# Performance work log

Hardware: AMD Instinct MI355X
Metric: run time of the kernel (lower is better)

Reference implementation:

```python
import jax, jax.numpy as jnp
import numpy as np

B, T9, N, C = 2048, 9, 62, 10   # batch, graph_num, node_num, dim_in
TT = 8                           # conv steps t=1..8
D = 62                           # TLSGCN dim_out (== node_num, required by GRU input_size)
ED = 3                           # emb_dim
K = 2                            # link_len
P = 100                          # zigzag persistence-image side
H = 62                           # GRU hidden size (BGI dim_out)


def setup_inputs() -> dict:
    key = jax.random.key(0)
    ks = jax.random.split(key, 12)
    s = 0.1
    return {
        "x": jax.random.normal(ks[0], (B, T9, N, C), jnp.float32),
        "zigzag_PI": jax.random.uniform(ks[1], (B, P, P), dtype=jnp.float32),
        "node_embeddings": jax.random.normal(ks[2], (N, ED), jnp.float32),
        "Wp": jax.random.normal(ks[3], (TT, ED, K, C, D), jnp.float32) * s,
        "bp": jax.random.normal(ks[4], (TT, ED, D), jnp.float32) * s,
        "Tparam": jax.random.normal(ks[5], (TT, T9), jnp.float32),
        "Wz": jax.random.normal(ks[6], (TT, P * P), jnp.float32) * 0.01,
        "W_ih": jax.random.normal(ks[7], (3 * H, D), jnp.float32) * s,
        "W_hh": jax.random.normal(ks[8], (3 * H, H), jnp.float32) * s,
        "b_ih": jnp.zeros((3 * H,), jnp.float32),
        "b_hh": jnp.zeros((3 * H,), jnp.float32),
        "W1": jax.random.normal(ks[9], (256, N), jnp.float32) * s,
        "b1": jnp.zeros((256,), jnp.float32),
        "W2": jax.random.normal(ks[10], (3, 256), jnp.float32) * s,
        "b2": jnp.zeros((3,), jnp.float32),
    }


def reference(x, zigzag_PI, node_embeddings, Wp, bp, Tparam, Wz,
              W_ih, W_hh, b_ih, b_hh, W1, b1, W2, b2):
    # --- TLSGCN graph diffusion conv, vectorized over the 8 per-step modules ---
    A = jax.nn.softmax(jax.nn.relu(node_embeddings @ node_embeddings.T), axis=1)  # [N,N]
    S = jnp.stack([jnp.eye(N, dtype=x.dtype), A], axis=0)                          # [K,N,N]
    w = jnp.einsum('ne,tekco->tnkco', node_embeddings, Wp)                         # [TT,N,K,C,D]
    b = jnp.einsum('ne,teo->tno', node_embeddings, bp)                             # [TT,N,D]
    xg = jnp.einsum('knm,btmc->btknc', S, x[:, 1:, :, :])                          # [B,TT,K,N,C]
    x_gconv = jnp.einsum('btknc,tnkco->btno', xg, w) + b[None]                     # [B,TT,N,D]
    # temporal window: step t attends over its first t frames (window_len = t)
    tmask = jnp.arange(T9)[None, :] < jnp.arange(1, TT + 1)[:, None]               # [TT,T9]
    alpha = jax.nn.softmax(jnp.where(tmask, Tparam, -jnp.inf), axis=1)             # [TT,T9]
    xw = jnp.einsum('bsnc,ts->btnc', x, alpha)                                     # [B,TT,N,C]
    x_wconv = jnp.einsum('btnc,tnco->btno', xw, w[:, :, 0])                        # [B,TT,N,D]
    # zigzag persistence-image topological gate (per step)
    zz = jax.nn.sigmoid(jnp.einsum('bp,tp->bt', zigzag_PI.reshape(B, -1), Wz))     # [B,TT]
    h = zz[:, :, None, None] * x_gconv + x_wconv                                   # [B,TT,N,D]
    h = jnp.where(jnp.isnan(h) | jnp.isinf(h), jnp.zeros((), h.dtype), h)
    # --- shared GRU applied per node: fold nodes into the batch dim ---
    seq = h.transpose(1, 0, 2, 3).reshape(TT, B * N, D)                            # [TT, B*N, D]

    def cell(hprev, xt):
        gi = xt @ W_ih.T + b_ih
        gh = hprev @ W_hh.T + b_hh
        ir, iz, inn = jnp.split(gi, 3, axis=-1)
        hr, hz, hn = jnp.split(gh, 3, axis=-1)
        r = jax.nn.sigmoid(ir + hr)
        zg = jax.nn.sigmoid(iz + hz)
        ng = jnp.tanh(inn + r * hn)
        hnew = (1.0 - zg) * ng + zg * hprev
        return hnew, None

    h0 = jnp.zeros((B * N, H), seq.dtype)
    hT, _ = jax.lax.scan(cell, h0, seq)        # final hidden == output at last step
    out = hT.reshape(B, N, H).sum(axis=2)      # [B, N]
    out = jax.nn.relu(out @ W1.T + b1)         # [B, 256]
    out = jax.nn.relu(out @ W2.T + b2)         # [B, 3]
    return out
```

## Files before the change

### kernel.cpp

```cpp
#include <hip/hip_runtime.h>

typedef unsigned short u16;
typedef _Float16 f16;
typedef __attribute__((ext_vector_type(8))) _Float16 h8v;
typedef __attribute__((ext_vector_type(4))) float f4v;

#define SC_RZ (-1.44269504f)
#define SC_N  (2.88539008f)

__device__ __forceinline__ u16 f2h_bits(float f){
  f16 h = (f16)f;
  return __builtin_bit_cast(u16, h);
}
__device__ __forceinline__ float sigmf(float x){
  return __builtin_amdgcn_rcpf(1.f + __expf(-x));
}

__global__ __launch_bounds__(64) void k_prepA(
    const float* __restrict__ E, const float* __restrict__ Tp,
    float* __restrict__ A, float* __restrict__ alpha)
{
  const int n = blockIdx.x, tid = threadIdx.x;
  if (n < 62){
    float e0 = E[n*3], e1 = E[n*3+1], e2 = E[n*3+2];
    float s = -1e30f;
    if (tid < 62){
      float d = e0*E[tid*3] + e1*E[tid*3+1] + e2*E[tid*3+2];
      s = d > 0.f ? d : 0.f;
    }
    float mx = s;
    #pragma unroll
    for (int off = 1; off < 64; off <<= 1) mx = fmaxf(mx, __shfl_xor(mx, off));
    float e = (tid < 62) ? __expf(s - mx) : 0.f;
    float sum = e;
    #pragma unroll
    for (int off = 1; off < 64; off <<= 1) sum += __shfl_xor(sum, off);
    if (tid < 62) A[n*62 + tid] = e / sum;
  } else {
    if (tid < 8){
      int t = tid;
      float mx = -1e30f;
      for (int s = 0; s <= t; ++s) mx = fmaxf(mx, Tp[t*9+s]);
      float sum = 0.f;
      for (int s = 0; s <= t; ++s) sum += __expf(Tp[t*9+s] - mx);
      float inv = 1.f / sum;
      for (int s = 0; s < 9; ++s)
        alpha[t*9+s] = (s <= t) ? __expf(Tp[t*9+s] - mx) * inv : 0.f;
    }
  }
}

__global__ __launch_bounds__(256) void k_wpad(
    const float* __restrict__ Whh, const float* __restrict__ bih,
    const float* __restrict__ bhh, u16* __restrict__ WhhH)
{
  int i = blockIdx.x*256 + threadIdx.x;
  if (i >= 12288) return;
  int row = i >> 6, k = i & 63, g = row >> 6, jj = row & 63;
  float sc = (g == 2) ? SC_N : SC_RZ;
  float vh = 0.f;
  if (jj < 62){
    if (k < 62) vh = Whh[(g*62+jj)*62 + k];
    else if (k == 62) vh = (g < 2) ? (bih[g*62+jj] + bhh[g*62+jj]) : bhh[124+jj];
  }
  WhhH[i] = f2h_bits(vh * sc);
}

__global__ __launch_bounds__(256) void k_m2(
    const float* __restrict__ E, const float* __restrict__ Wp,
    const float* __restrict__ bp, const float* __restrict__ Wih,
    const float* __restrict__ bih, u16* __restrict__ M2)
{
  const int bid = blockIdx.x;
  const int t = bid / 62, n = bid % 62, tid = threadIdx.x;
  __shared__ float w2s[1240];
  __shared__ float bias[62];
  const float e0 = E[n*3], e1 = E[n*3+1], e2 = E[n*3+2];
  for (int i = tid; i < 1240; i += 256){
    int o = i / 20, k = i % 20, c = k >> 1, kl = k & 1;
    w2s[i] = e0*Wp[(((t*3+0)*2+kl)*10+c)*62 + o]
           + e1*Wp[(((t*3+1)*2+kl)*10+c)*62 + o]
           + e2*Wp[(((t*3+2)*2+kl)*10+c)*62 + o];
  }
  if (tid < 62)
    bias[tid] = e0*bp[(t*3+0)*62+tid] + e1*bp[(t*3+1)*62+tid]
              + e2*bp[(t*3+2)*62+tid];
  __syncthreads();
  for (int i = tid; i < 3072; i += 256){
    int col = i >> 4, d = i & 15, g = col >> 6, jj = col & 63;
    float sc = (g == 2) ? SC_N : SC_RZ;
    unsigned outw = 0;
    if (jj < 62){
      const float* wr = Wih + (g*62+jj)*62;
      if (d < 10){
        int k0 = 2*d;
        float v0 = 0.f, v1 = 0.f;
        for (int o = 0; o < 62; ++o){
          float w = wr[o];
          v0 += w * w2s[o*20 + k0];
          v1 += w * w2s[o*20 + k0 + 1];
        }
        outw = (unsigned)f2h_bits(v0*sc) | ((unsigned)f2h_bits(v1*sc) << 16);
      } else if (d == 10){
        float v0 = 0.f;
        for (int o = 0; o < 62; ++o) v0 += wr[o]*bias[o];
        float v1 = (g == 2) ? bih[124+jj] : 0.f;
        outw = (unsigned)f2h_bits(v0*sc) | ((unsigned)f2h_bits(v1*sc) << 16);
      }
    }
    ((unsigned*)M2)[((size_t)bid*192 + col)*16 + d] = outw;
  }
}

__global__ __launch_bounds__(256) void k_zz(
    const float* __restrict__ PI, const float* __restrict__ Wz,
    float* __restrict__ zzO)
{
  const int b0 = blockIdx.x*4, tid = threadIdx.x;
  float acc[32];
  #pragma unroll
  for (int i = 0; i < 32; ++i) acc[i] = 0.f;
  const float4* p0 = (const float4*)(PI + (size_t)(b0+0)*10000);
  const float4* p1 = (const float4*)(PI + (size_t)(b0+1)*10000);
  const float4* p2 = (const float4*)(PI + (size_t)(b0+2)*10000);
  const float4* p3 = (const float4*)(PI + (size_t)(b0+3)*10000);
  const float4* wz4 = (const float4*)Wz;
  for (int p = tid; p < 2500; p += 256){
    float4 x0 = p0[p], x1 = p1[p], x2 = p2[p], x3 = p3[p];
    #pragma unroll
    for (int t = 0; t < 8; ++t){
      float4 w = wz4[t*2500 + p];
      acc[t*4+0] += x0.x*w.x + x0.y*w.y + x0.z*w.z + x0.w*w.w;
      acc[t*4+1] += x1.x*w.x + x1.y*w.y + x1.z*w.z + x1.w*w.w;
      acc[t*4+2] += x2.x*w.x + x2.y*w.y + x2.z*w.z + x2.w*w.w;
      acc[t*4+3] += x3.x*w.x + x3.y*w.y + x3.z*w.z + x3.w*w.w;
    }
  }
  __shared__ float red[128];
  int lane = tid & 63, wid = tid >> 6;
  #pragma unroll
  for (int i = 0; i < 32; ++i){
    float v = acc[i];
    v += __shfl_xor(v, 1);  v += __shfl_xor(v, 2);  v += __shfl_xor(v, 4);
    v += __shfl_xor(v, 8);  v += __shfl_xor(v, 16); v += __shfl_xor(v, 32);
    if (lane == 0) red[i*4 + wid] = v;
  }
  __syncthreads();
  if (tid < 32){
    float s = red[tid*4] + red[tid*4+1] + red[tid*4+2] + red[tid*4+3];
    int t = tid >> 2, bq = tid & 3;
    zzO[t*2048 + b0 + bq] = sigmf(s);
  }
}

__global__ __launch_bounds__(256) void k_u(
    const float* __restrict__ x, const float* __restrict__ A,
    const float* __restrict__ alpha, const float* __restrict__ zz,
    u16* __restrict__ U01)
{
  const int b = blockIdx.x, tid = threadIdx.x;
  __shared__ float xs[5580];
  __shared__ f16 xT[80*72];
  __shared__ f16 A16[64*72];
  __shared__ f16 xg[64*80];
  __shared__ float al[72];
  __shared__ float zzb[8];

  const float* pxb = x + (size_t)b*5580;
  const float4* px4 = (const float4*)pxb;
  for (int i = tid; i < 1395; i += 256) ((float4*)xs)[i] = px4[i];
  for (int i = tid; i < 3844; i += 256){
    int n = i / 62, m = i % 62;
    A16[n*72 + m] = (f16)A[i];
  }
  for (int i = tid; i < 640; i += 256) A16[(i/10)*72 + 62 + (i%10)] = (f16)0.f;
  for (int i = tid; i < 124; i += 256) A16[(62 + i/62)*72 + (i%62)] = (f16)0.f;
  for (int i = tid; i < 4960; i += 256){
    int s1 = i / 620, r = i % 620, m = r / 10, c = r % 10;
    xT[(s1*10 + c)*72 + m] = (f16)pxb[620 + i];
  }
  for (int i = tid; i < 800; i += 256) xT[(i/10)*72 + 62 + (i%10)] = (f16)0.f;
  if (tid < 72) al[tid] = alpha[tid];
  if (tid < 8) zzb[tid] = zz[tid*2048 + b];
  __syncthreads();

  {
    const int w_id = tid >> 6, lane = tid & 63, ln = lane & 15, hi = lane >> 4;
    h8v af0 = *(const h8v*)&A16[(w_id*16 + ln)*72 + hi*8];
    h8v af1 = *(const h8v*)&A16[(w_id*16 + ln)*72 + 32 + hi*8];
    f4v Z4 = {0.f, 0.f, 0.f, 0.f};
    #pragma unroll
    for (int Nt = 0; Nt < 5; ++Nt){
      h8v bf0 = *(const h8v*)&xT[(Nt*16 + ln)*72 + hi*8];
      h8v bf1 = *(const h8v*)&xT[(Nt*16 + ln)*72 + 32 + hi*8];
      f4v acc = __builtin_amdgcn_mfma_f32_16x16x32_f16(af0, bf0, Z4, 0,0,0);
      acc = __builtin_amdgcn_mfma_f32_16x16x32_f16(af1, bf1, acc, 0,0,0);
      #pragma unroll
      for (int rg = 0; rg < 4; ++rg)
        xg[(w_id*16 + hi*4 + rg)*80 + Nt*16 + ln] = (f16)acc[rg];
    }
  }
  __syncthreads();

  const int t = tid >> 5, nq = (tid >> 1) & 15, ch = tid & 1;
  const int n0 = nq*4, c0 = ch*5;
  float alr[9];
  #pragma unroll
  for (int s = 0; s < 9; ++s) alr[s] = al[t*9+s];
  const float z = zzb[t];
  const unsigned zpack = (unsigned)f2h_bits(z) | (0x3C00u << 16);
  #pragma unroll
  for (int i = 0; i < 4; ++i){
    int n = n0 + i;
    if (n < 62){
      unsigned pk[5];
      #pragma unroll
      for (int c = 0; c < 5; ++c){
        int cc = c0 + c;
        float xw = 0.f;
        #pragma unroll
        for (int s = 0; s < 9; ++s) xw += alr[s]*xs[s*620 + n*10 + cc];
        float u0 = z*xs[(t+1)*620 + n*10 + cc] + xw;
        float u1 = z*(float)xg[n*80 + t*10 + cc];
        pk[c] = (unsigned)f2h_bits(u0) | ((unsigned)f2h_bits(u1) << 16);
      }
      unsigned* dst = (unsigned*)(U01 + ((size_t)(t*62 + n)*2048 + b)*32);
      #pragma unroll
      for (int c = 0; c < 5; ++c) dst[c0 + c] = pk[c];
      if (ch == 0){ dst[10] = zpack; dst[12] = 0; dst[13] = 0; }
      else        { dst[11] = 0;     dst[14] = 0; dst[15] = 0; }
    }
  }
}

__global__ __launch_bounds__(256, 3) void k_gru(
    const u16* __restrict__ U01, const u16* __restrict__ M2,
    const u16* __restrict__ WhhH, float* __restrict__ outSum)
{
  __shared__ f16 Hs[2][32*72];
  __shared__ float red[128];

  const int tid = threadIdx.x;
  int bid = blockIdx.x;
  bid = (bid & 7)*496 + (bid >> 3);
  const int n_idx = bid >> 6;
  const int b0 = (bid & 63) << 5;
  const int lane = tid & 63;
  const int w_id = tid >> 6;
  const int ln = lane & 15;
  const int hi = lane >> 4;
  const int j = w_id*16 + ln;

  h8v whhF[3][2];
  #pragma unroll
  for (int g = 0; g < 3; ++g)
    #pragma unroll
    for (int ks = 0; ks < 2; ++ks)
      whhF[g][ks] = *(const h8v*)(const void*)(WhhH + (g*64 + j)*64 + ks*32 + hi*8);

  for (int i = tid; i < 2304; i += 256){
    f16 v = ((i % 72) == 62) ? (f16)1.f : (f16)0.f;
    Hs[0][i] = v; Hs[1][i] = v;
  }

  const u16* pU = U01 + ((size_t)n_idx*2048 + b0)*32;
  const u16* pM = M2 + (size_t)n_idx*192*32;
  const int oU0 = ln*32 + hi*8;
  const int oU1 = (16 + ln)*32 + hi*8;
  const int oM0 = j*32 + hi*8;
  const int oM1 = (64 + j)*32 + hi*8;
  const int oM2 = (128 + j)*32 + hi*8;
  const size_t TSU = (size_t)62*2048*32;
  const size_t TSM = (size_t)62*192*32;

  h8v uA0 = *(const h8v*)(const void*)(pU + oU0);
  h8v uA1 = *(const h8v*)(const void*)(pU + oU1);
  h8v mA0 = *(const h8v*)(const void*)(pM + oM0);
  h8v mA1 = *(const h8v*)(const void*)(pM + oM1);
  h8v mA2 = *(const h8v*)(const void*)(pM + oM2);
  h8v uB0, uB1, mB0, mB1, mB2;

  float h_reg[8];
  #pragma unroll
  for (int i = 0; i < 8; ++i) h_reg[i] = 0.f;
  __syncthreads();

  const f4v Z4 = {0.f, 0.f, 0.f, 0.f};
  #pragma unroll
  for (int t = 0; t < 8; ++t){
    const int p = t & 1;
    if (t < 7){
      const u16* qU = pU + (size_t)(t+1)*TSU;
      const u16* qM = pM + (size_t)(t+1)*TSM;
      uB0 = *(const h8v*)(const void*)(qU + oU0);
      uB1 = *(const h8v*)(const void*)(qU + oU1);
      mB0 = *(const h8v*)(const void*)(qM + oM0);
      mB1 = *(const h8v*)(const void*)(qM + oM1);
      mB2 = *(const h8v*)(const void*)(qM + oM2);
    }
    h8v hf00 = *(const h8v*)&Hs[p][ln*72 + hi*8];
    h8v hf01 = *(const h8v*)&Hs[p][ln*72 + 32 + hi*8];
    h8v hf10 = *(const h8v*)&Hs[p][(16+ln)*72 + hi*8];
    h8v hf11 = *(const h8v*)&Hs[p][(16+ln)*72 + 32 + hi*8];

    f4v ar[2], az[2], axn[2], ahn[2];
    ar[0]  = __builtin_amdgcn_mfma_f32_16x16x32_f16(hf00, whhF[0][0], Z4, 0,0,0);
    ar[0]  = __builtin_amdgcn_mfma_f32_16x16x32_f16(hf01, whhF[0][1], ar[0], 0,0,0);
    ar[0]  = __builtin_amdgcn_mfma_f32_16x16x32_f16(uA0, mA0, ar[0], 0,0,0);
    ar[1]  = __builtin_amdgcn_mfma_f32_16x16x32_f16(hf10, whhF[0][0], Z4, 0,0,0);
    ar[1]  = __builtin_amdgcn_mfma_f32_16x16x32_f16(hf11, whhF[0][1], ar[1], 0,0,0);
    ar[1]  = __builtin_amdgcn_mfma_f32_16x16x32_f16(uA1, mA0, ar[1], 0,0,0);
    az[0]  = __builtin_amdgcn_mfma_f32_16x16x32_f16(hf00, whhF[1][0], Z4, 0,0,0);
    az[0]  = __builtin_amdgcn_mfma_f32_16x16x32_f16(hf01, whhF[1][1], az[0], 0,0,0);
    az[0]  = __builtin_amdgcn_mfma_f32_16x16x32_f16(uA0, mA1, az[0], 0,0,0);
    az[1]  = __builtin_amdgcn_mfma_f32_16x16x32_f16(hf10, whhF[1][0], Z4, 0,0,0);
    az[1]  = __builtin_amdgcn_mfma_f32_16x16x32_f16(hf11, whhF[1][1], az[1], 0,0,0);
    az[1]  = __builtin_amdgcn_mfma_f32_16x16x32_f16(uA1, mA1, az[1], 0,0,0);
    ahn[0] = __builtin_amdgcn_mfma_f32_16x16x32_f16(hf00, whhF[2][0], Z4, 0,0,0);
    ahn[0] = __builtin_amdgcn_mfma_f32_16x16x32_f16(hf01, whhF[2][1], ahn[0], 0,0,0);
    ahn[1] = __builtin_amdgcn_mfma_f32_16x16x32_f16(hf10, whhF[2][0], Z4, 0,0,0);
    ahn[1] = __builtin_amdgcn_mfma_f32_16x16x32_f16(hf11, whhF[2][1], ahn[1], 0,0,0);
    axn[0] = __builtin_amdgcn_mfma_f32_16x16x32_f16(uA0, mA2, Z4, 0,0,0);
    axn[1] = __builtin_amdgcn_mfma_f32_16x16x32_f16(uA1, mA2, Z4, 0,0,0);

    const bool last = (t == 7);
    #pragma unroll
    for (int mi = 0; mi < 2; ++mi)
      #pragma unroll
      for (int rg = 0; rg < 4; ++rg){
        float r  = __builtin_amdgcn_rcpf(1.f + exp2f(ar[mi][rg]));
        float zg = __builtin_amdgcn_rcpf(1.f + exp2f(az[mi][rg]));
        float yn = axn[mi][rg] + r*ahn[mi][rg];
        float ng = fmaf(-2.f, __builtin_amdgcn_rcpf(1.f + exp2f(yn)), 1.f);
        int idx = mi*4 + rg;
        float hnew = ng + zg*(h_reg[idx] - ng);
        h_reg[idx] = hnew;
        if (!last && j < 62)
          Hs[p^1][(mi*16 + hi*4 + rg)*72 + j] = (f16)hnew;
      }
    uA0 = uB0; uA1 = uB1; mA0 = mB0; mA1 = mB1; mA2 = mB2;
    __syncthreads();
  }

  #pragma unroll
  for (int mi = 0; mi < 2; ++mi)
    #pragma unroll
    for (int rg = 0; rg < 4; ++rg){
      float v = (j < 62) ? h_reg[mi*4 + rg] : 0.f;
      v += __shfl_xor(v, 1); v += __shfl_xor(v, 2);
      v += __shfl_xor(v, 4); v += __shfl_xor(v, 8);
      if (ln == 0) red[w_id*32 + mi*16 + hi*4 + rg] = v;
    }
  __syncthreads();
  if (tid < 32)
    outSum[(size_t)n_idx*2048 + b0 + tid] =
        red[tid] + red[32+tid] + red[64+tid] + red[96+tid];
}

__global__ __launch_bounds__(256) void k_mlp(
    const float* __restrict__ outSum,
    const float* __restrict__ W1, const float* __restrict__ b1,
    const float* __restrict__ W2, const float* __restrict__ b2,
    float* __restrict__ out)
{
  const int b0 = blockIdx.x*8, tid = threadIdx.x;
  __shared__ float W1s[15872];
  __shared__ float vec[8][62];
  __shared__ float o1[8][256];
  for (int i = tid; i < 15872; i += 256) W1s[i] = W1[i];
  for (int i = tid; i < 496; i += 256){
    int n = i >> 3, bl = i & 7;
    vec[bl][n] = outSum[(size_t)n*2048 + b0 + bl];
  }
  __syncthreads();
  {
    float a[8];
    #pragma unroll
    for (int bl = 0; bl < 8; ++bl) a[bl] = b1[tid];
    for (int n = 0; n < 62; ++n){
      float w = W1s[tid*62 + n];
      #pragma unroll
      for (int bl = 0; bl < 8; ++bl) a[bl] += w * vec[bl][n];
    }
    #pragma unroll
    for (int bl = 0; bl < 8; ++bl) o1[bl][tid] = fmaxf(a[bl], 0.f);
  }
  __syncthreads();
  if (tid < 24){
    int bl = tid / 3, o = tid % 3;
    float s = b2[o];
    for (int k = 0; k < 256; ++k) s += o1[bl][k]*W2[o*256 + k];
    out[(b0+bl)*3 + o] = fmaxf(s, 0.f);
  }
}

extern "C" void kernel_launch(void* const* d_in, const int* in_sizes, int n_in,
                              void* d_out, int out_size, void* d_ws, size_t ws_size,
                              hipStream_t stream)
{
  const float* x   = (const float*)d_in[0];
  const float* PI  = (const float*)d_in[1];
  const float* E   = (const float*)d_in[2];
  const float* Wp  = (const float*)d_in[3];
  const float* bp  = (const float*)d_in[4];
  const float* Tp  = (const float*)d_in[5];
  const float* Wz  = (const float*)d_in[6];
  const float* Wih = (const float*)d_in[7];
  const float* Whh = (const float*)d_in[8];
  const float* bih = (const float*)d_in[9];
  const float* bhh = (const float*)d_in[10];
  const float* W1  = (const float*)d_in[11];
  const float* b1  = (const float*)d_in[12];
  const float* W2  = (const float*)d_in[13];
  const float* b2  = (const float*)d_in[14];
  float* out = (float*)d_out;

  char* ws = (char*)d_ws;
  size_t off = 0;
  auto take = [&](size_t bytes)->char*{
    char* p = ws + off; off = (off + bytes + 255) & ~(size_t)255; return p;
  };
  float* pA     = (float*)take(3844*4);
  float* palpha = (float*)take(72*4);
  float* pzz    = (float*)take(16384*4);
  u16*   pWhhH  = (u16*)take(12288*2);
  u16*   pM2    = (u16*)take((size_t)496*192*32*2);
  u16*   pU01   = (u16*)take((size_t)496*2048*32*2);
  float* pos    = (float*)take((size_t)126976*4);

  k_prepA<<<63, 64, 0, stream>>>(E, Tp, pA, palpha);
  k_wpad<<<48, 256, 0, stream>>>(Whh, bih, bhh, pWhhH);
  k_m2<<<496, 256, 0, stream>>>(E, Wp, bp, Wih, bih, pM2);
  k_zz<<<512, 256, 0, stream>>>(PI, Wz, pzz);
  k_u<<<2048, 256, 0, stream>>>(x, pA, palpha, pzz, pU01);
  k_gru<<<3968, 256, 0, stream>>>(pU01, pM2, pWhhH, pos);
  k_mlp<<<256, 256, 0, stream>>>(pos, W1, b1, W2, b2, out);
}
```

Measured before the change: 204.8 us.

## Restructure GRU kernel to per-wave independent rows, drop block syncs, shrink U buffer

The GRU kernel is rewritten so each wave owns 16 batch rows and computes all 64 hidden outputs itself, with weights as the A operand. The hidden state now stays in per-wave LDS and in packed half registers, which removes the block-wide __syncthreads per timestep and the cross-wave reduction. The U01 staging buffer row stride drops from 32 to 24 halves to cut memory traffic, and the two prep kernels are merged into one launch. The cost is more registers (occupancy hint lowered to 2), M2 fragments reloaded each step, and the hidden state carried between steps in fp16 rather than fp32, which may change accuracy.

```diff
diff --git a/kernel.cpp b/kernel.cpp
--- a/kernel.cpp
+++ b/kernel.cpp
@@ -1,7 +1,9 @@
 #include <hip/hip_runtime.h>
 
 typedef unsigned short u16;
+typedef unsigned int u32;
 typedef _Float16 f16;
+typedef __attribute__((ext_vector_type(2))) _Float16 h2v;
 typedef __attribute__((ext_vector_type(8))) _Float16 h8v;
 typedef __attribute__((ext_vector_type(4))) float f4v;
 
@@ -16,27 +18,32 @@
   return __builtin_amdgcn_rcpf(1.f + __expf(-x));
 }
 
-__global__ __launch_bounds__(64) void k_prepA(
+__global__ __launch_bounds__(256) void k_prep(
     const float* __restrict__ E, const float* __restrict__ Tp,
-    float* __restrict__ A, float* __restrict__ alpha)
-{
-  const int n = blockIdx.x, tid = threadIdx.x;
-  if (n < 62){
-    float e0 = E[n*3], e1 = E[n*3+1], e2 = E[n*3+2];
-    float s = -1e30f;
-    if (tid < 62){
-      float d = e0*E[tid*3] + e1*E[tid*3+1] + e2*E[tid*3+2];
-      s = d > 0.f ? d : 0.f;
-    }
-    float mx = s;
-    #pragma unroll
-    for (int off = 1; off < 64; off <<= 1) mx = fmaxf(mx, __shfl_xor(mx, off));
-    float e = (tid < 62) ? __expf(s - mx) : 0.f;
-    float sum = e;
-    #pragma unroll
-    for (int off = 1; off < 64; off <<= 1) sum += __shfl_xor(sum, off);
-    if (tid < 62) A[n*62 + tid] = e / sum;
-  } else {
+    const float* __restrict__ Whh, const float* __restrict__ bih,
+    const float* __restrict__ bhh,
+    float* __restrict__ A, float* __restrict__ alpha, u16* __restrict__ WhhH)
+{
+  const int bid = blockIdx.x, tid = threadIdx.x;
+  if (bid < 62){
+    if (tid < 64){
+      const int n = bid;
+      float e0 = E[n*3], e1 = E[n*3+1], e2 = E[n*3+2];
+      float s = -1e30f;
+      if (tid < 62){
+        float d = e0*E[tid*3] + e1*E[tid*3+1] + e2*E[tid*3+2];
+        s = d > 0.f ? d : 0.f;
+      }
+      float mx = s;
+      #pragma unroll
+      for (int off = 1; off < 64; off <<= 1) mx = fmaxf(mx, __shfl_xor(mx, off));
+      float e = (tid < 62) ? __expf(s - mx) : 0.f;
+      float sum = e;
+      #pragma unroll
+      for (int off = 1; off < 64; off <<= 1) sum += __shfl_xor(sum, off);
+      if (tid < 62) A[n*62 + tid] = e / sum;
+    }
+  } else if (bid == 62){
     if (tid < 8){
       int t = tid;
       float mx = -1e30f;
@@ -47,23 +54,19 @@
       for (int s = 0; s < 9; ++s)
         alpha[t*9+s] = (s <= t) ? __expf(Tp[t*9+s] - mx) * inv : 0.f;
     }
-  }
-}
-
-__global__ __launch_bounds__(256) void k_wpad(
-    const float* __restrict__ Whh, const float* __restrict__ bih,
-    const float* __restrict__ bhh, u16* __restrict__ WhhH)
-{
-  int i = blockIdx.x*256 + threadIdx.x;
-  if (i >= 12288) return;
-  int row = i >> 6, k = i & 63, g = row >> 6, jj = row & 63;
-  float sc = (g == 2) ? SC_N : SC_RZ;
-  float vh = 0.f;
-  if (jj < 62){
-    if (k < 62) vh = Whh[(g*62+jj)*62 + k];
-    else if (k == 62) vh = (g < 2) ? (bih[g*62+jj] + bhh[g*62+jj]) : bhh[124+jj];
-  }
-  WhhH[i] = f2h_bits(vh * sc);
+  } else {
+    int i = (bid - 63)*256 + tid;
+    if (i < 12288){
+      int row = i >> 6, k = i & 63, g = row >> 6, jj = row & 63;
+      float sc = (g == 2) ? SC_N : SC_RZ;
+      float vh = 0.f;
+      if (jj < 62){
+        if (k < 62) vh = Whh[(g*62+jj)*62 + k];
+        else if (k == 62) vh = (g < 2) ? (bih[g*62+jj] + bhh[g*62+jj]) : bhh[124+jj];
+      }
+      WhhH[i] = f2h_bits(vh * sc);
+    }
+  }
 }
 
 __global__ __launch_bounds__(256) void k_m2(
@@ -224,137 +227,131 @@
         float u1 = z*(float)xg[n*80 + t*10 + cc];
         pk[c] = (unsigned)f2h_bits(u0) | ((unsigned)f2h_bits(u1) << 16);
       }
-      unsigned* dst = (unsigned*)(U01 + ((size_t)(t*62 + n)*2048 + b)*32);
+      unsigned* dst = (unsigned*)(U01 + ((size_t)(t*62 + n)*2048 + b)*24);
       #pragma unroll
       for (int c = 0; c < 5; ++c) dst[c0 + c] = pk[c];
-      if (ch == 0){ dst[10] = zpack; dst[12] = 0; dst[13] = 0; }
-      else        { dst[11] = 0;     dst[14] = 0; dst[15] = 0; }
-    }
-  }
-}
-
-__global__ __launch_bounds__(256, 3) void k_gru(
+      if (ch == 0) dst[10] = zpack; else dst[11] = 0;
+    }
+  }
+}
+
+__global__ __launch_bounds__(256, 2) void k_gru(
     const u16* __restrict__ U01, const u16* __restrict__ M2,
     const u16* __restrict__ WhhH, float* __restrict__ outSum)
 {
-  __shared__ f16 Hs[2][32*72];
-  __shared__ float red[128];
+  __shared__ f16 Ht[4][16*72];
 
   const int tid = threadIdx.x;
   int bid = blockIdx.x;
-  bid = (bid & 7)*496 + (bid >> 3);
-  const int n_idx = bid >> 6;
-  const int b0 = (bid & 63) << 5;
+  bid = (bid & 7)*248 + (bid >> 3);
+  const int n_idx = bid >> 5;
+  const int w_id = tid >> 6;
+  const int row0 = (bid & 31)*64 + w_id*16;
   const int lane = tid & 63;
-  const int w_id = tid >> 6;
   const int ln = lane & 15;
   const int hi = lane >> 4;
-  const int j = w_id*16 + ln;
-
-  h8v whhF[3][2];
+
+  f16* Hw = &Ht[w_id][0];
+
+  h8v whhA[3][4][2];
   #pragma unroll
   for (int g = 0; g < 3; ++g)
     #pragma unroll
-    for (int ks = 0; ks < 2; ++ks)
-      whhF[g][ks] = *(const h8v*)(const void*)(WhhH + (g*64 + j)*64 + ks*32 + hi*8);
-
-  for (int i = tid; i < 2304; i += 256){
-    f16 v = ((i % 72) == 62) ? (f16)1.f : (f16)0.f;
-    Hs[0][i] = v; Hs[1][i] = v;
-  }
-
-  const u16* pU = U01 + ((size_t)n_idx*2048 + b0)*32;
-  const u16* pM = M2 + (size_t)n_idx*192*32;
-  const int oU0 = ln*32 + hi*8;
-  const int oU1 = (16 + ln)*32 + hi*8;
-  const int oM0 = j*32 + hi*8;
-  const int oM1 = (64 + j)*32 + hi*8;
-  const int oM2 = (128 + j)*32 + hi*8;
-  const size_t TSU = (size_t)62*2048*32;
+    for (int jt = 0; jt < 4; ++jt)
+      #pragma unroll
+      for (int kc = 0; kc < 2; ++kc)
+        whhA[g][jt][kc] = *(const h8v*)(const void*)(
+            WhhH + (g*64 + jt*16 + ln)*64 + kc*32 + hi*8);
+
+  {
+    u32* wp = (u32*)(Hw + ln*72);
+    #pragma unroll
+    for (int jt = 0; jt < 4; ++jt)
+      #pragma unroll
+      for (int half = 0; half < 2; ++half){
+        u32 v = (jt==3 && half==1 && hi==3) ? 0x00003C00u : 0u;
+        wp[8*jt + 2*hi + half] = v;
+      }
+  }
+
+  const size_t TSU = (size_t)62*2048*24;
   const size_t TSM = (size_t)62*192*32;
-
-  h8v uA0 = *(const h8v*)(const void*)(pU + oU0);
-  h8v uA1 = *(const h8v*)(const void*)(pU + oU1);
-  h8v mA0 = *(const h8v*)(const void*)(pM + oM0);
-  h8v mA1 = *(const h8v*)(const void*)(pM + oM1);
-  h8v mA2 = *(const h8v*)(const void*)(pM + oM2);
-  h8v uB0, uB1, mB0, mB1, mB2;
-
-  float h_reg[8];
-  #pragma unroll
-  for (int i = 0; i < 8; ++i) h_reg[i] = 0.f;
-  __syncthreads();
-
+  const u16* pU = U01 + ((size_t)n_idx*2048 + row0)*24 + ln*24 + hi*8;
+  const u16* pM = M2 + (size_t)n_idx*192*32 + ln*32 + hi*8;
+
+  u32 hpack[8];
+  #pragma unroll
+  for (int i = 0; i < 8; ++i) hpack[i] = 0;
+
+  h8v uBuf[2];
+  uBuf[0] = (hi < 3) ? *(const h8v*)(const void*)(pU) : (h8v){};
+  float sum = 0.f;
   const f4v Z4 = {0.f, 0.f, 0.f, 0.f};
+
   #pragma unroll
   for (int t = 0; t < 8; ++t){
-    const int p = t & 1;
-    if (t < 7){
-      const u16* qU = pU + (size_t)(t+1)*TSU;
-      const u16* qM = pM + (size_t)(t+1)*TSM;
-      uB0 = *(const h8v*)(const void*)(qU + oU0);
-      uB1 = *(const h8v*)(const void*)(qU + oU1);
-      mB0 = *(const h8v*)(const void*)(qM + oM0);
-      mB1 = *(const h8v*)(const void*)(qM + oM1);
-      mB2 = *(const h8v*)(const void*)(qM + oM2);
-    }
-    h8v hf00 = *(const h8v*)&Hs[p][ln*72 + hi*8];
-    h8v hf01 = *(const h8v*)&Hs[p][ln*72 + 32 + hi*8];
-    h8v hf10 = *(const h8v*)&Hs[p][(16+ln)*72 + hi*8];
-    h8v hf11 = *(const h8v*)&Hs[p][(16+ln)*72 + 32 + hi*8];
-
-    f4v ar[2], az[2], axn[2], ahn[2];
-    ar[0]  = __builtin_amdgcn_mfma_f32_16x16x32_f16(hf00, whhF[0][0], Z4, 0,0,0);
-    ar[0]  = __builtin_amdgcn_mfma_f32_16x16x32_f16(hf01, whhF[0][1], ar[0], 0,0,0);
-    ar[0]  = __builtin_amdgcn_mfma_f32_16x16x32_f16(uA0, mA0, ar[0], 0,0,0);
-    ar[1]  = __builtin_amdgcn_mfma_f32_16x16x32_f16(hf10, whhF[0][0], Z4, 0,0,0);
-    ar[1]  = __builtin_amdgcn_mfma_f32_16x16x32_f16(hf11, whhF[0][1], ar[1], 0,0,0);
-    ar[1]  = __builtin_amdgcn_mfma_f32_16x16x32_f16(uA1, mA0, ar[1], 0,0,0);
-    az[0]  = __builtin_amdgcn_mfma_f32_16x16x32_f16(hf00, whhF[1][0], Z4, 0,0,0);
-    az[0]  = __builtin_amdgcn_mfma_f32_16x16x32_f16(hf01, whhF[1][1], az[0], 0,0,0);
-    az[0]  = __builtin_amdgcn_mfma_f32_16x16x32_f16(uA0, mA1, az[0], 0,0,0);
-    az[1]  = __builtin_amdgcn_mfma_f32_16x16x32_f16(hf10, whhF[1][0], Z4, 0,0,0);
-    az[1]  = __builtin_amdgcn_mfma_f32_16x16x32_f16(hf11, whhF[1][1], az[1], 0,0,0);
-    az[1]  = __builtin_amdgcn_mfma_f32_16x16x32_f16(uA1, mA1, az[1], 0,0,0);
-    ahn[0] = __builtin_amdgcn_mfma_f32_16x16x32_f16(hf00, whhF[2][0], Z4, 0,0,0);
-    ahn[0] = __builtin_amdgcn_mfma_f32_16x16x32_f16(hf01, whhF[2][1], ahn[0], 0,0,0);
-    ahn[1] = __builtin_amdgcn_mfma_f32_16x16x32_f16(hf10, whhF[2][0], Z4, 0,0,0);
-    ahn[1] = __builtin_amdgcn_mfma_f32_16x16x32_f16(hf11, whhF[2][1], ahn[1], 0,0,0);
-    axn[0] = __builtin_amdgcn_mfma_f32_16x16x32_f16(uA0, mA2, Z4, 0,0,0);
-    axn[1] = __builtin_amdgcn_mfma_f32_16x16x32_f16(uA1, mA2, Z4, 0,0,0);
+    h8v hb0 = *(const h8v*)&Hw[ln*72 + hi*8];
+    h8v hb1 = *(const h8v*)&Hw[ln*72 + 32 + hi*8];
+    h8v m2A[3][4];
+    #pragma unroll
+    for (int g = 0; g < 3; ++g)
+      #pragma unroll
+      for (int jt = 0; jt < 4; ++jt)
+        m2A[g][jt] = *(const h8v*)(const void*)(
+            pM + (size_t)t*TSM + (g*64 + jt*16)*32);
+    if (t < 7)
+      uBuf[(t+1)&1] = (hi < 3) ?
+          *(const h8v*)(const void*)(pU + (size_t)(t+1)*TSU) : (h8v){};
+    h8v u = uBuf[t&1];
+
+    f4v ar[4], az[4], axn[4], ahn[4];
+    #pragma unroll
+    for (int jt = 0; jt < 4; ++jt){
+      ar[jt]  = __builtin_amdgcn_mfma_f32_16x16x32_f16(whhA[0][jt][0], hb0, Z4, 0,0,0);
+      ar[jt]  = __builtin_amdgcn_mfma_f32_16x16x32_f16(whhA[0][jt][1], hb1, ar[jt], 0,0,0);
+      az[jt]  = __builtin_amdgcn_mfma_f32_16x16x32_f16(whhA[1][jt][0], hb0, Z4, 0,0,0);
+      az[jt]  = __builtin_amdgcn_mfma_f32_16x16x32_f16(whhA[1][jt][1], hb1, az[jt], 0,0,0);
+      ahn[jt] = __builtin_amdgcn_mfma_f32_16x16x32_f16(whhA[2][jt][0], hb0, Z4, 0,0,0);
+      ahn[jt] = __builtin_amdgcn_mfma_f32_16x16x32_f16(whhA[2][jt][1], hb1, ahn[jt], 0,0,0);
+      ar[jt]  = __builtin_amdgcn_mfma_f32_16x16x32_f16(m2A[0][jt], u, ar[jt], 0,0,0);
+      az[jt]  = __builtin_amdgcn_mfma_f32_16x16x32_f16(m2A[1][jt], u, az[jt], 0,0,0);
+      axn[jt] = __builtin_amdgcn_mfma_f32_16x16x32_f16(m2A[2][jt], u, Z4, 0,0,0);
+    }
 
     const bool last = (t == 7);
-    #pragma unroll
-    for (int mi = 0; mi < 2; ++mi)
+    u32* wp = (u32*)(Hw + ln*72);
+    #pragma unroll
+    for (int jt = 0; jt < 4; ++jt){
+      float hn4[4];
       #pragma unroll
       for (int rg = 0; rg < 4; ++rg){
-        float r  = __builtin_amdgcn_rcpf(1.f + exp2f(ar[mi][rg]));
-        float zg = __builtin_amdgcn_rcpf(1.f + exp2f(az[mi][rg]));
-        float yn = axn[mi][rg] + r*ahn[mi][rg];
+        float r  = __builtin_amdgcn_rcpf(1.f + exp2f(ar[jt][rg]));
+        float zg = __builtin_amdgcn_rcpf(1.f + exp2f(az[jt][rg]));
+        float yn = fmaf(r, ahn[jt][rg], axn[jt][rg]);
         float ng = fmaf(-2.f, __builtin_amdgcn_rcpf(1.f + exp2f(yn)), 1.f);
-        int idx = mi*4 + rg;
-        float hnew = ng + zg*(h_reg[idx] - ng);
-        h_reg[idx] = hnew;
-        if (!last && j < 62)
-          Hs[p^1][(mi*16 + hi*4 + rg)*72 + j] = (f16)hnew;
-      }
-    uA0 = uB0; uA1 = uB1; mA0 = mB0; mA1 = mB1; mA2 = mB2;
-    __syncthreads();
-  }
-
-  #pragma unroll
-  for (int mi = 0; mi < 2; ++mi)
-    #pragma unroll
-    for (int rg = 0; rg < 4; ++rg){
-      float v = (j < 62) ? h_reg[mi*4 + rg] : 0.f;
-      v += __shfl_xor(v, 1); v += __shfl_xor(v, 2);
-      v += __shfl_xor(v, 4); v += __shfl_xor(v, 8);
-      if (ln == 0) red[w_id*32 + mi*16 + hi*4 + rg] = v;
-    }
-  __syncthreads();
-  if (tid < 32)
-    outSum[(size_t)n_idx*2048 + b0 + tid] =
-        red[tid] + red[32+tid] + red[64+tid] + red[96+tid];
+        u16 hb16 = (u16)(hpack[jt*2 + (rg>>1)] >> ((rg&1)*16));
+        float h = (float)__builtin_bit_cast(f16, hb16);
+        float hnew = fmaf(zg, h - ng, ng);
+        hn4[rg] = hnew;
+      }
+      if (last){
+        sum += hn4[0] + hn4[1];
+        if (!(jt == 3 && hi == 3)) sum += hn4[2] + hn4[3];
+      } else {
+        u32 p0 = __builtin_bit_cast(u32, __builtin_amdgcn_cvt_pkrtz(hn4[0], hn4[1]));
+        u32 p1 = __builtin_bit_cast(u32, __builtin_amdgcn_cvt_pkrtz(hn4[2], hn4[3]));
+        if (jt == 3 && hi == 3) p1 = 0x00003C00u;
+        hpack[jt*2] = p0; hpack[jt*2+1] = p1;
+        wp[8*jt + 2*hi + 0] = p0;
+        wp[8*jt + 2*hi + 1] = p1;
+      }
+    }
+  }
+
+  sum += __shfl_xor(sum, 16);
+  sum += __shfl_xor(sum, 32);
+  if (lane < 16)
+    outSum[(size_t)n_idx*2048 + row0 + ln] = sum;
 }
 
 __global__ __launch_bounds__(256) void k_mlp(
@@ -425,14 +422,13 @@
   float* pzz    = (float*)take(16384*4);
   u16*   pWhhH  = (u16*)take(12288*2);
   u16*   pM2    = (u16*)take((size_t)496*192*32*2);
-  u16*   pU01   = (u16*)take((size_t)496*2048*32*2);
+  u16*   pU01   = (u16*)take((size_t)496*2048*24*2);
   float* pos    = (float*)take((size_t)126976*4);
 
-  k_prepA<<<63, 64, 0, stream>>>(E, Tp, pA, palpha);
-  k_wpad<<<48, 256, 0, stream>>>(Whh, bih, bhh, pWhhH);
+  k_prep<<<111, 256, 0, stream>>>(E, Tp, Whh, bih, bhh, pA, palpha, pWhhH);
   k_m2<<<496, 256, 0, stream>>>(E, Wp, bp, Wih, bih, pM2);
   k_zz<<<512, 256, 0, stream>>>(PI, Wz, pzz);
   k_u<<<2048, 256, 0, stream>>>(x, pA, palpha, pzz, pU01);
-  k_gru<<<3968, 256, 0, stream>>>(pU01, pM2, pWhhH, pos);
+  k_gru<<<1984, 256, 0, stream>>>(pU01, pM2, pWhhH, pos);
   k_mlp<<<256, 256, 0, stream>>>(pos, W1, b1, W2, b2, out);
 }
```

Result: slower. 225.1 us (+9.9%).

## Shrink U01 row stride to 24 halves, deepen U prefetch, merge prep kernels

Applied to the files above, without the earlier changes.

Each U01 row is shrunk from 32 to 24 f16 values, dropping the zero padding. The GRU kernel then loads only the first three 8-wide chunks, with hi==3 lanes using zeros held in registers, which cuts the traffic of the largest intermediate tensor by a quarter. The U operand prefetch becomes a 3-slot ring that loads two timesteps ahead. The two small prep kernels are merged into one launch to save launch overhead, and a few expressions are rewritten as explicit fmaf. The deeper ring adds register pressure under launch bounds of 3 blocks per SIMD.

```diff
diff --git a/kernel.cpp b/kernel.cpp
--- a/kernel.cpp
+++ b/kernel.cpp
@@ -1,6 +1,7 @@
 #include <hip/hip_runtime.h>
 
 typedef unsigned short u16;
+typedef unsigned int u32;
 typedef _Float16 f16;
 typedef __attribute__((ext_vector_type(8))) _Float16 h8v;
 typedef __attribute__((ext_vector_type(4))) float f4v;
@@ -16,27 +17,32 @@
   return __builtin_amdgcn_rcpf(1.f + __expf(-x));
 }
 
-__global__ __launch_bounds__(64) void k_prepA(
+__global__ __launch_bounds__(256) void k_prep(
     const float* __restrict__ E, const float* __restrict__ Tp,
-    float* __restrict__ A, float* __restrict__ alpha)
-{
-  const int n = blockIdx.x, tid = threadIdx.x;
-  if (n < 62){
-    float e0 = E[n*3], e1 = E[n*3+1], e2 = E[n*3+2];
-    float s = -1e30f;
-    if (tid < 62){
-      float d = e0*E[tid*3] + e1*E[tid*3+1] + e2*E[tid*3+2];
-      s = d > 0.f ? d : 0.f;
-    }
-    float mx = s;
-    #pragma unroll
-    for (int off = 1; off < 64; off <<= 1) mx = fmaxf(mx, __shfl_xor(mx, off));
-    float e = (tid < 62) ? __expf(s - mx) : 0.f;
-    float sum = e;
-    #pragma unroll
-    for (int off = 1; off < 64; off <<= 1) sum += __shfl_xor(sum, off);
-    if (tid < 62) A[n*62 + tid] = e / sum;
-  } else {
+    const float* __restrict__ Whh, const float* __restrict__ bih,
+    const float* __restrict__ bhh,
+    float* __restrict__ A, float* __restrict__ alpha, u16* __restrict__ WhhH)
+{
+  const int bid = blockIdx.x, tid = threadIdx.x;
+  if (bid < 62){
+    if (tid < 64){
+      const int n = bid;
+      float e0 = E[n*3], e1 = E[n*3+1], e2 = E[n*3+2];
+      float s = -1e30f;
+      if (tid < 62){
+        float d = e0*E[tid*3] + e1*E[tid*3+1] + e2*E[tid*3+2];
+        s = d > 0.f ? d : 0.f;
+      }
+      float mx = s;
+      #pragma unroll
+      for (int off = 1; off < 64; off <<= 1) mx = fmaxf(mx, __shfl_xor(mx, off));
+      float e = (tid < 62) ? __expf(s - mx) : 0.f;
+      float sum = e;
+      #pragma unroll
+      for (int off = 1; off < 64; off <<= 1) sum += __shfl_xor(sum, off);
+      if (tid < 62) A[n*62 + tid] = e / sum;
+    }
+  } else if (bid == 62){
     if (tid < 8){
       int t = tid;
       float mx = -1e30f;
@@ -47,23 +53,19 @@
       for (int s = 0; s < 9; ++s)
         alpha[t*9+s] = (s <= t) ? __expf(Tp[t*9+s] - mx) * inv : 0.f;
     }
-  }
-}
-
-__global__ __launch_bounds__(256) void k_wpad(
-    const float* __restrict__ Whh, const float* __restrict__ bih,
-    const float* __restrict__ bhh, u16* __restrict__ WhhH)
-{
-  int i = blockIdx.x*256 + threadIdx.x;
-  if (i >= 12288) return;
-  int row = i >> 6, k = i & 63, g = row >> 6, jj = row & 63;
-  float sc = (g == 2) ? SC_N : SC_RZ;
-  float vh = 0.f;
-  if (jj < 62){
-    if (k < 62) vh = Whh[(g*62+jj)*62 + k];
-    else if (k == 62) vh = (g < 2) ? (bih[g*62+jj] + bhh[g*62+jj]) : bhh[124+jj];
-  }
-  WhhH[i] = f2h_bits(vh * sc);
+  } else {
+    int i = (bid - 63)*256 + tid;
+    if (i < 12288){
+      int row = i >> 6, k = i & 63, g = row >> 6, jj = row & 63;
+      float sc = (g == 2) ? SC_N : SC_RZ;
+      float vh = 0.f;
+      if (jj < 62){
+        if (k < 62) vh = Whh[(g*62+jj)*62 + k];
+        else if (k == 62) vh = (g < 2) ? (bih[g*62+jj] + bhh[g*62+jj]) : bhh[124+jj];
+      }
+      WhhH[i] = f2h_bits(vh * sc);
+    }
+  }
 }
 
 __global__ __launch_bounds__(256) void k_m2(
@@ -224,11 +226,10 @@
         float u1 = z*(float)xg[n*80 + t*10 + cc];
         pk[c] = (unsigned)f2h_bits(u0) | ((unsigned)f2h_bits(u1) << 16);
       }
-      unsigned* dst = (unsigned*)(U01 + ((size_t)(t*62 + n)*2048 + b)*32);
+      unsigned* dst = (unsigned*)(U01 + ((size_t)(t*62 + n)*2048 + b)*24);
       #pragma unroll
       for (int c = 0; c < 5; ++c) dst[c0 + c] = pk[c];
-      if (ch == 0){ dst[10] = zpack; dst[12] = 0; dst[13] = 0; }
-      else        { dst[11] = 0;     dst[14] = 0; dst[15] = 0; }
+      if (ch == 0) dst[10] = zpack; else dst[11] = 0;
     }
   }
 }
@@ -263,37 +264,45 @@
     Hs[0][i] = v; Hs[1][i] = v;
   }
 
-  const u16* pU = U01 + ((size_t)n_idx*2048 + b0)*32;
+  const size_t TSU = (size_t)62*2048*24;
+  const size_t TSM = (size_t)62*192*32;
+  const u16* pU = U01 + ((size_t)n_idx*2048 + b0)*24;
   const u16* pM = M2 + (size_t)n_idx*192*32;
-  const int oU0 = ln*32 + hi*8;
-  const int oU1 = (16 + ln)*32 + hi*8;
+  const int oU0 = ln*24 + hi*8;
+  const int oU1 = (16 + ln)*24 + hi*8;
   const int oM0 = j*32 + hi*8;
   const int oM1 = (64 + j)*32 + hi*8;
   const int oM2 = (128 + j)*32 + hi*8;
-  const size_t TSU = (size_t)62*2048*32;
-  const size_t TSM = (size_t)62*192*32;
-
-  h8v uA0 = *(const h8v*)(const void*)(pU + oU0);
-  h8v uA1 = *(const h8v*)(const void*)(pU + oU1);
+
+  h8v uF[3][2];
+  #pragma unroll
+  for (int s = 0; s < 3; ++s){ uF[s][0] = (h8v){}; uF[s][1] = (h8v){}; }
+  auto ldU = [&](int t, int s){
+    if (hi < 3){
+      uF[s][0] = *(const h8v*)(const void*)(pU + (size_t)t*TSU + oU0);
+      uF[s][1] = *(const h8v*)(const void*)(pU + (size_t)t*TSU + oU1);
+    }
+  };
+  ldU(0, 0); ldU(1, 1);
   h8v mA0 = *(const h8v*)(const void*)(pM + oM0);
   h8v mA1 = *(const h8v*)(const void*)(pM + oM1);
   h8v mA2 = *(const h8v*)(const void*)(pM + oM2);
-  h8v uB0, uB1, mB0, mB1, mB2;
+  h8v mB0, mB1, mB2;
 
   float h_reg[8];
   #pragma unroll
   for (int i = 0; i < 8; ++i) h_reg[i] = 0.f;
+  const bool jok = (j < 62);
   __syncthreads();
 
   const f4v Z4 = {0.f, 0.f, 0.f, 0.f};
   #pragma unroll
   for (int t = 0; t < 8; ++t){
     const int p = t & 1;
+    const int su = t % 3;
+    if (t < 6) ldU(t+2, (t+2)%3);
     if (t < 7){
-      const u16* qU = pU + (size_t)(t+1)*TSU;
       const u16* qM = pM + (size_t)(t+1)*TSM;
-      uB0 = *(const h8v*)(const void*)(qU + oU0);
-      uB1 = *(const h8v*)(const void*)(qU + oU1);
       mB0 = *(const h8v*)(const void*)(qM + oM0);
       mB1 = *(const h8v*)(const void*)(qM + oM1);
       mB2 = *(const h8v*)(const void*)(qM + oM2);
@@ -302,26 +311,27 @@
     h8v hf01 = *(const h8v*)&Hs[p][ln*72 + 32 + hi*8];
     h8v hf10 = *(const h8v*)&Hs[p][(16+ln)*72 + hi*8];
     h8v hf11 = *(const h8v*)&Hs[p][(16+ln)*72 + 32 + hi*8];
+    h8v u0 = uF[su][0], u1 = uF[su][1];
 
     f4v ar[2], az[2], axn[2], ahn[2];
     ar[0]  = __builtin_amdgcn_mfma_f32_16x16x32_f16(hf00, whhF[0][0], Z4, 0,0,0);
     ar[0]  = __builtin_amdgcn_mfma_f32_16x16x32_f16(hf01, whhF[0][1], ar[0], 0,0,0);
-    ar[0]  = __builtin_amdgcn_mfma_f32_16x16x32_f16(uA0, mA0, ar[0], 0,0,0);
+    ar[0]  = __builtin_amdgcn_mfma_f32_16x16x32_f16(u0, mA0, ar[0], 0,0,0);
     ar[1]  = __builtin_amdgcn_mfma_f32_16x16x32_f16(hf10, whhF[0][0], Z4, 0,0,0);
     ar[1]  = __builtin_amdgcn_mfma_f32_16x16x32_f16(hf11, whhF[0][1], ar[1], 0,0,0);
-    ar[1]  = __builtin_amdgcn_mfma_f32_16x16x32_f16(uA1, mA0, ar[1], 0,0,0);
+    ar[1]  = __builtin_amdgcn_mfma_f32_16x16x32_f16(u1, mA0, ar[1], 0,0,0);
     az[0]  = __builtin_amdgcn_mfma_f32_16x16x32_f16(hf00, whhF[1][0], Z4, 0,0,0);
     az[0]  = __builtin_amdgcn_mfma_f32_16x16x32_f16(hf01, whhF[1][1], az[0], 0,0,0);
-    az[0]  = __builtin_amdgcn_mfma_f32_16x16x32_f16(uA0, mA1, az[0], 0,0,0);
+    az[0]  = __builtin_amdgcn_mfma_f32_16x16x32_f16(u0, mA1, az[0], 0,0,0);
     az[1]  = __builtin_amdgcn_mfma_f32_16x16x32_f16(hf10, whhF[1][0], Z4, 0,0,0);
     az[1]  = __builtin_amdgcn_mfma_f32_16x16x32_f16(hf11, whhF[1][1], az[1], 0,0,0);
-    az[1]  = __builtin_amdgcn_mfma_f32_16x16x32_f16(uA1, mA1, az[1], 0,0,0);
+    az[1]  = __builtin_amdgcn_mfma_f32_16x16x32_f16(u1, mA1, az[1], 0,0,0);
     ahn[0] = __builtin_amdgcn_mfma_f32_16x16x32_f16(hf00, whhF[2][0], Z4, 0,0,0);
     ahn[0] = __builtin_amdgcn_mfma_f32_16x16x32_f16(hf01, whhF[2][1], ahn[0], 0,0,0);
     ahn[1] = __builtin_amdgcn_mfma_f32_16x16x32_f16(hf10, whhF[2][0], Z4, 0,0,0);
     ahn[1] = __builtin_amdgcn_mfma_f32_16x16x32_f16(hf11, whhF[2][1], ahn[1], 0,0,0);
-    axn[0] = __builtin_amdgcn_mfma_f32_16x16x32_f16(uA0, mA2, Z4, 0,0,0);
-    axn[1] = __builtin_amdgcn_mfma_f32_16x16x32_f16(uA1, mA2, Z4, 0,0,0);
+    axn[0] = __builtin_amdgcn_mfma_f32_16x16x32_f16(u0, mA2, Z4, 0,0,0);
+    axn[1] = __builtin_amdgcn_mfma_f32_16x16x32_f16(u1, mA2, Z4, 0,0,0);
 
     const bool last = (t == 7);
     #pragma unroll
@@ -330,15 +340,15 @@
       for (int rg = 0; rg < 4; ++rg){
         float r  = __builtin_amdgcn_rcpf(1.f + exp2f(ar[mi][rg]));
         float zg = __builtin_amdgcn_rcpf(1.f + exp2f(az[mi][rg]));
-        float yn = axn[mi][rg] + r*ahn[mi][rg];
+        float yn = fmaf(r, ahn[mi][rg], axn[mi][rg]);
         float ng = fmaf(-2.f, __builtin_amdgcn_rcpf(1.f + exp2f(yn)), 1.f);
         int idx = mi*4 + rg;
-        float hnew = ng + zg*(h_reg[idx] - ng);
+        float hnew = fmaf(zg, h_reg[idx] - ng, ng);
         h_reg[idx] = hnew;
-        if (!last && j < 62)
+        if (!last && jok)
           Hs[p^1][(mi*16 + hi*4 + rg)*72 + j] = (f16)hnew;
       }
-    uA0 = uB0; uA1 = uB1; mA0 = mB0; mA1 = mB1; mA2 = mB2;
+    mA0 = mB0; mA1 = mB1; mA2 = mB2;
     __syncthreads();
   }
 
@@ -346,7 +356,7 @@
   for (int mi = 0; mi < 2; ++mi)
     #pragma unroll
     for (int rg = 0; rg < 4; ++rg){
-      float v = (j < 62) ? h_reg[mi*4 + rg] : 0.f;
+      float v = jok ? h_reg[mi*4 + rg] : 0.f;
       v += __shfl_xor(v, 1); v += __shfl_xor(v, 2);
       v += __shfl_xor(v, 4); v += __shfl_xor(v, 8);
       if (ln == 0) red[w_id*32 + mi*16 + hi*4 + rg] = v;
@@ -425,11 +435,10 @@
   float* pzz    = (float*)take(16384*4);
   u16*   pWhhH  = (u16*)take(12288*2);
   u16*   pM2    = (u16*)take((size_t)496*192*32*2);
-  u16*   pU01   = (u16*)take((size_t)496*2048*32*2);
+  u16*   pU01   = (u16*)take((size_t)496*2048*24*2);
   float* pos    = (float*)take((size_t)126976*4);
 
-  k_prepA<<<63, 64, 0, stream>>>(E, Tp, pA, palpha);
-  k_wpad<<<48, 256, 0, stream>>>(Whh, bih, bhh, pWhhH);
+  k_prep<<<111, 256, 0, stream>>>(E, Tp, Whh, bih, bhh, pA, palpha, pWhhH);
   k_m2<<<496, 256, 0, stream>>>(E, Wp, bp, Wih, bih, pM2);
   k_zz<<<512, 256, 0, stream>>>(PI, Wz, pzz);
   k_u<<<2048, 256, 0, stream>>>(x, pA, palpha, pzz, pU01);
```

Result: no change. 204.6 us (-0.1%).
